# Kernel tuning notes

Measured on AMD Instinct MI355X. Metric: run time of the kernel, lower is better.

Reference implementation:

```python
import jax, jax.numpy as jnp
import numpy as np

HEAD_DIM = 128
NUM_Q_HEAD = 32
NUM_KV_HEAD = 8
GROUP_SIZE = 128
EPS = 1e-5
WINDOW = 512
CAP = 50.0
CLIP_L, CLIP_R = -0.01, 1.01
SCALE = 1.0 / np.sqrt(HEAD_DIM)
NEG = -1e9


def group_rmsnorm(x, gamma, gsz, eps):
    # x: [B, S, H]; per-group RMS over contiguous chunks of size gsz, then learned scale
    b, s, h = x.shape
    xg = x.reshape(b, s, h // gsz, gsz)
    rms = jnp.sqrt(jnp.mean(xg * xg, axis=-1, keepdims=True) + eps)
    return (xg / rms).reshape(b, s, h) * gamma


def setup_inputs() -> dict:
    key = jax.random.key(0)
    k1, k2, k3, k4, k5 = jax.random.split(key, 5)
    B, S = 2, 2048
    q = jax.random.normal(k1, (B, S, NUM_Q_HEAD, HEAD_DIM), dtype=jnp.float32)
    k = jax.random.normal(k2, (B, S, NUM_KV_HEAD, HEAD_DIM), dtype=jnp.float32)
    v = jax.random.normal(k3, (B, S, NUM_KV_HEAD, HEAD_DIM), dtype=jnp.float32)
    # GroupRMSNorm weights ~ U(init_range) = U(-1, 1)
    gamma_q = jax.random.uniform(k4, (NUM_Q_HEAD * HEAD_DIM,), dtype=jnp.float32, minval=-1.0, maxval=1.0)
    gamma_k = jax.random.uniform(k5, (NUM_KV_HEAD * HEAD_DIM,), dtype=jnp.float32, minval=-1.0, maxval=1.0)
    return {"q": q, "k": k, "v": v, "gamma_q": gamma_q, "gamma_k": gamma_k}


def reference(q, k, v, gamma_q, gamma_k):
    B, Sq, Hq, D = q.shape
    Sk, Hkv = k.shape[1], k.shape[2]
    # QK GroupRMSNorm on flattened hidden dim
    qn = group_rmsnorm(q.reshape(B, Sq, Hq * D), gamma_q, GROUP_SIZE, EPS).reshape(B, Sq, Hq, D)
    kn = group_rmsnorm(k.reshape(B, Sk, Hkv * D), gamma_k, GROUP_SIZE, EPS).reshape(B, Sk, Hkv, D)
    # GQA: repeat_interleave kv heads to match q heads
    rep = Hq // Hkv
    kr = jnp.repeat(kn, rep, axis=2)
    vr = jnp.repeat(v, rep, axis=2)
    # scores: [B, H, Sq, Sk]
    logits = jnp.einsum('bqhd,bkhd->bhqk', qn, kr) * SCALE
    # softmax capping (temperature path skipped when cap is set)
    logits = jnp.tanh(logits / CAP) * CAP
    # causal + sliding-window mask (aligned at sequence end)
    i = jnp.arange(Sq)[:, None]
    j = jnp.arange(Sk)[None, :]
    pos = i + (Sk - Sq)
    allowed = (j <= pos) & (pos - j <= WINDOW)
    logits = jnp.where(allowed, logits, NEG)
    probs = jax.nn.softmax(logits.astype(jnp.float32), axis=-1)
    # softmax clipping: clamp(probs * (r - l) + l, 0, 1)
    probs = jnp.clip(probs * (CLIP_R - CLIP_L) + CLIP_L, 0.0, 1.0)
    # output: [B, Sq, H, D]
    o = jnp.einsum('bhqk,bkhd->bqhd', probs.astype(q.dtype), vr)
    return o
```

## Files before the change

### kernel.cpp

```cpp
#include <hip/hip_runtime.h>

#define SEQ     2048
#define NQH     32
#define NKV     8
#define HD      128
#define WINDOW  512
#define QT      64
#define EPS_F   1e-5f
#define CQ2     0.12752981793f
#define PSTR    72

#define KN_OFF  0ull
#define VT_OFF  8388608ull

#define ROWPAT(r, hg) ((((r) & 3) + 8 * ((r) >> 2)) + 4 * (hg))

#define WAIT_BAR_4() asm volatile("s_waitcnt vmcnt(4)\n\ts_barrier" ::: "memory")
#define WAIT_BAR_0() asm volatile("s_waitcnt vmcnt(0)\n\ts_barrier" ::: "memory")
#define WAIT_BARL_4() asm volatile("s_waitcnt vmcnt(4) lgkmcnt(0)\n\ts_barrier" ::: "memory")
#define WAIT_BARL_0() asm volatile("s_waitcnt vmcnt(0) lgkmcnt(0)\n\ts_barrier" ::: "memory")
#define LGKM_BAR()  asm volatile("s_waitcnt lgkmcnt(0)\n\ts_barrier" ::: "memory")

using bf16x8 = __attribute__((ext_vector_type(8))) __bf16;
using f32x16 = __attribute__((ext_vector_type(16))) float;

__device__ __forceinline__ void dma16(const void* g, void* l) {
    __builtin_amdgcn_global_load_lds(
        (const __attribute__((address_space(1))) unsigned int*)g,
        (__attribute__((address_space(3))) unsigned int*)l, 16, 0, 0);
}

__global__ __launch_bounds__(256)
void prep(const float* __restrict__ k, const float* __restrict__ v,
          const float* __restrict__ gk,
          __bf16* __restrict__ kn, __bf16* __restrict__ vt)
{
    __shared__ __align__(16) __bf16 sT[HD * 72];
    const int blk = blockIdx.x;
    const int tid = threadIdx.x;
    if (blk < 512) {
        const int l16  = tid & 15;
        const int rsub = tid >> 4;
        #pragma unroll
        for (int it = 0; it < 4; it++) {
            const int row = blk * 64 + it * 16 + rsub;
            const float* src = k + (size_t)row * HD + l16 * 8;
            const float* g   = gk + (row & 7) * HD + l16 * 8;
            float4 a  = *(const float4*)(src);
            float4 b4 = *(const float4*)(src + 4);
            float ss = a.x*a.x + a.y*a.y + a.z*a.z + a.w*a.w
                     + b4.x*b4.x + b4.y*b4.y + b4.z*b4.z + b4.w*b4.w;
            ss += __shfl_xor(ss, 1); ss += __shfl_xor(ss, 2);
            ss += __shfl_xor(ss, 4); ss += __shfl_xor(ss, 8);
            const float rs = rsqrtf(ss * (1.f / 128.f) + EPS_F);
            float4 g0 = *(const float4*)(g);
            float4 g1 = *(const float4*)(g + 4);
            bf16x8 o;
            o[0] = (__bf16)(a.x  * rs * g0.x);  o[1] = (__bf16)(a.y  * rs * g0.y);
            o[2] = (__bf16)(a.z  * rs * g0.z);  o[3] = (__bf16)(a.w  * rs * g0.w);
            o[4] = (__bf16)(b4.x * rs * g1.x);  o[5] = (__bf16)(b4.y * rs * g1.y);
            o[6] = (__bf16)(b4.z * rs * g1.z);  o[7] = (__bf16)(b4.w * rs * g1.w);
            *(bf16x8*)(kn + (size_t)row * HD + l16 * 8) = o;
        }
    } else {
        const int blk2 = blk - 512;
        const int st  = blk2 & 31;
        const int kvh = (blk2 >> 5) & 7;
        const int b   = blk2 >> 8;
        const int s0  = st * 64;
        {
            const int r  = tid >> 2;
            const int q4 = tid & 3;
            const float* src = v + ((size_t)(b * SEQ + s0 + r) * NKV + kvh) * HD;
            #pragma unroll
            for (int u = 0; u < 8; u++) {
                const int d0 = q4 * 4 + u * 16;
                float4 x = *(const float4*)(src + d0);
                sT[(d0 + 0) * 72 + r] = (__bf16)x.x;
                sT[(d0 + 1) * 72 + r] = (__bf16)x.y;
                sT[(d0 + 2) * 72 + r] = (__bf16)x.z;
                sT[(d0 + 3) * 72 + r] = (__bf16)x.w;
            }
        }
        __syncthreads();
        {
            const int c     = tid & 7;
            const int dbase = tid >> 3;
            __bf16* dst = vt + ((size_t)(b * NKV + kvh) * HD) * SEQ + s0;
            #pragma unroll
            for (int i = 0; i < 4; i++) {
                const int d = dbase + i * 32;
                bf16x8 w = *(const bf16x8*)&sT[d * 72 + c * 8];
                *(bf16x8*)(dst + (size_t)d * SEQ + c * 8) = w;
            }
        }
    }
}

#define WRITEP(TTW, BUF) do {                                                  \
    _Pragma("unroll")                                                          \
    for (int half_ = 0; half_ < 2; half_++) {                                  \
        _Pragma("unroll")                                                      \
        for (int j_ = 0; j_ < 8; j_++) {                                       \
            const int r_ = half_ * 8 + j_;                                     \
            const float ee_ = (float)ec[TTW][half_][j_];                       \
            const float f_ = fminf(fmaxf(fmaf(ee_, ar[r_], -0.01f), 0.f), 1.f);\
            sP[BUF][(mhalf * 32 + ROWPAT(r_, hg)) * PSTR + krow] = (__bf16)f_; \
        }                                                                      \
    }                                                                          \
} while (0)

__global__ __launch_bounds__(256, 2)
void swa_main(const float* __restrict__ q, const __bf16* __restrict__ kn,
              const __bf16* __restrict__ vt, const float* __restrict__ gq,
              float* __restrict__ out)
{
    __shared__ __align__(16) __bf16 sKV[3][QT * HD];
    __shared__ __align__(16) __bf16 sP[2][QT * PSTR];
    __shared__ float sLp[2][QT];
    __shared__ float sInvL[QT];

    const int wg0  = blockIdx.x;
    const int xcd  = wg0 & 7;
    const int gi   = wg0 >> 3;
    const int pair = xcd * 2 + (gi >> 7);
    const int rr_  = gi & 127;
    const int qt   = rr_ & 31;
    const int h    = (pair & 7) * 4 + (rr_ >> 5);
    const int b    = pair >> 3;
    const int kvh  = pair & 7;
    const int i0   = qt * QT;
    const int tid  = threadIdx.x;
    const int lane = tid & 63;
    const int wave = tid >> 6;
    const int mhalf = wave & 1;
    const int nhalf = wave >> 1;
    const int m    = lane & 31;
    const int hg   = lane >> 5;

    const char* k_src[4];  const char* v_src[4];
    int kq_off[4];  int v_off[4];
    {
        const char* kn_head = (const char*)kn + ((size_t)b * SEQ * NKV + kvh) * 256;
        const char* vt_head = (const char*)vt + ((size_t)(b * NKV + kvh) * HD) * (SEQ * 2);
        #pragma unroll
        for (int i = 0; i < 4; i++) {
            const int chunk = wave * 4 + i;
            {
                const int r    = chunk * 4 + (lane >> 4);
                const int cpos = lane & 15;
                const int c    = (cpos & 8) | ((cpos ^ r) & 7);
                k_src[i]  = kn_head + (size_t)r * (NKV * HD * 2) + c * 16;
                kq_off[i] = chunk * 1024;
            }
            {
                const int r    = chunk * 8 + (lane >> 3);
                const int cpos = lane & 7;
                const int c    = cpos ^ (r & 7);
                v_src[i] = vt_head + (size_t)r * (SEQ * 2) + c * 16;
                v_off[i] = chunk * 1024;
            }
        }
    }

    const int t_lo   = (i0 >= WINDOW ? (i0 - WINDOW) : 0) >> 6;
    const int t_hi   = i0 >> 6;
    const int ttbias = t_hi - 8;
    const int tt0    = t_lo - ttbias;
    const int krow   = nhalf * 32 + m;
    const size_t kstride = (size_t)64 * (NKV * HD * 2);

    {
        const size_t ko = (size_t)t_lo * kstride;
        char* dst0 = (char*)&sKV[t_lo % 3][0];
        #pragma unroll
        for (int i = 0; i < 4; i++) dma16(k_src[i] + ko, dst0 + kq_off[i]);
        if (t_lo < t_hi) {
            char* dst1 = (char*)&sKV[(t_lo + 1) % 3][0];
            #pragma unroll
            for (int i = 0; i < 4; i++) dma16(k_src[i] + ko + kstride, dst1 + kq_off[i]);
        }
    }

    bf16x8 qf[8];
    {
        const int qrow = i0 + mhalf * 32 + m;
        const float* qp = q + ((size_t)(b * SEQ + qrow) * NQH + h) * HD;
        float4 qb[16];
        float ss = 0.0f;
        #pragma unroll
        for (int kf = 0; kf < 8; kf++) {
            const int d0 = kf * 16 + hg * 8;
            float4 a  = *(const float4*)(qp + d0);
            float4 b4 = *(const float4*)(qp + d0 + 4);
            qb[kf * 2] = a; qb[kf * 2 + 1] = b4;
            ss += a.x*a.x + a.y*a.y + a.z*a.z + a.w*a.w
                + b4.x*b4.x + b4.y*b4.y + b4.z*b4.z + b4.w*b4.w;
        }
        ss += __shfl_xor(ss, 32);
        const float rs = rsqrtf(ss * (1.f / 128.f) + EPS_F) * CQ2;
        const float* gp = gq + h * HD;
        #pragma unroll
        for (int kf = 0; kf < 8; kf++) {
            const int d0 = kf * 16 + hg * 8;
            float4 g0 = *(const float4*)(gp + d0);
            float4 g1 = *(const float4*)(gp + d0 + 4);
            bf16x8 f;
            f[0] = (__bf16)(qb[kf*2].x   * rs * g0.x);
            f[1] = (__bf16)(qb[kf*2].y   * rs * g0.y);
            f[2] = (__bf16)(qb[kf*2].z   * rs * g0.z);
            f[3] = (__bf16)(qb[kf*2].w   * rs * g0.w);
            f[4] = (__bf16)(qb[kf*2+1].x * rs * g1.x);
            f[5] = (__bf16)(qb[kf*2+1].y * rs * g1.y);
            f[6] = (__bf16)(qb[kf*2+1].z * rs * g1.z);
            f[7] = (__bf16)(qb[kf*2+1].w * rs * g1.w);
            qf[kf] = f;
        }
    }

    float lacc[16];
    #pragma unroll
    for (int i = 0; i < 16; i++) lacc[i] = 0.f;
    bf16x8 ec[9][2];

    #pragma unroll
    for (int tt = 0; tt < 9; tt++) {
        const int t = ttbias + tt;
        if (t >= t_lo) {
            if (t < t_hi) { WAIT_BAR_4(); } else { WAIT_BAR_0(); }
            const __bf16* kb = &sKV[t % 3][0];
            bf16x8 bk[8];
            #pragma unroll
            for (int kf = 0; kf < 8; kf++) {
                const int cc  = kf * 2 + hg;
                const int pos = (cc & 8) | ((cc ^ krow) & 7);
                bk[kf] = *(const bf16x8*)(kb + krow * HD + pos * 8);
            }
            if (t + 2 <= t_hi) {
                const size_t ko = (size_t)(t + 2) * kstride;
                char* dstp = (char*)&sKV[(t + 2) % 3][0];
                #pragma unroll
                for (int i = 0; i < 4; i++) dma16(k_src[i] + ko, dstp + kq_off[i]);
            }
            f32x16 c0, c1;
            #pragma unroll
            for (int i = 0; i < 16; i++) { c0[i] = 0.f; c1[i] = 0.f; }
            __builtin_amdgcn_s_setprio(1);
            #pragma unroll
            for (int kf = 0; kf < 4; kf++) {
                c0 = __builtin_amdgcn_mfma_f32_32x32x16_bf16(qf[2*kf],   bk[2*kf],   c0, 0, 0, 0);
                c1 = __builtin_amdgcn_mfma_f32_32x32x16_bf16(qf[2*kf+1], bk[2*kf+1], c1, 0, 0, 0);
            }
            __builtin_amdgcn_s_setprio(0);

            const bool do_mask = (t == t_hi) || (t == t_lo && i0 >= WINDOW);
            const int kj = t * 64 + krow;
            float e[16];
            #pragma unroll
            for (int r = 0; r < 16; r++) {
                float ev = __builtin_amdgcn_exp2f(c0[r] + c1[r]);
                if (do_mask) {
                    const int qi = i0 + mhalf * 32 + ROWPAT(r, hg);
                    ev = ((unsigned)(qi - kj) <= WINDOW) ? ev : 0.f;
                }
                lacc[r] += ev;
                e[r] = ev;
            }
            bf16x8 p0v, p1v;
            #pragma unroll
            for (int j = 0; j < 8; j++) { p0v[j] = (__bf16)e[j]; p1v[j] = (__bf16)e[8 + j]; }
            ec[tt][0] = p0v;  ec[tt][1] = p1v;
        }
    }

    #pragma unroll
    for (int r = 0; r < 16; r++) {
        float l = lacc[r];
        l += __shfl_xor(l, 1);  l += __shfl_xor(l, 2);  l += __shfl_xor(l, 4);
        l += __shfl_xor(l, 8);  l += __shfl_xor(l, 16);
        lacc[r] = l;
    }
    if (m == 0) {
        #pragma unroll
        for (int r = 0; r < 16; r++)
            sLp[nhalf][mhalf * 32 + ROWPAT(r, hg)] = lacc[r];
    }
    LGKM_BAR();
    {
        const size_t vo = (size_t)t_lo * 128;
        char* dst0 = (char*)&sKV[t_lo % 3][0];
        #pragma unroll
        for (int i = 0; i < 4; i++) dma16(v_src[i] + vo, dst0 + v_off[i]);
        if (t_lo < t_hi) {
            char* dst1 = (char*)&sKV[(t_lo + 1) % 3][0];
            #pragma unroll
            for (int i = 0; i < 4; i++) dma16(v_src[i] + vo + 128, dst1 + v_off[i]);
        }
    }
    if (tid < QT) sInvL[tid] = __builtin_amdgcn_rcpf(sLp[0][tid] + sLp[1][tid]);
    LGKM_BAR();

    float ar[16];
    #pragma unroll
    for (int r = 0; r < 16; r++) ar[r] = 1.02f * sInvL[mhalf * 32 + ROWPAT(r, hg)];

    #pragma unroll
    for (int tt = 0; tt < 9; tt++) if (tt == tt0) WRITEP(tt, tt & 1);

    f32x16 o0, o1;
    #pragma unroll
    for (int i = 0; i < 16; i++) { o0[i] = 0.f; o1[i] = 0.f; }

    #pragma unroll
    for (int tt = 0; tt < 9; tt++) {
        const int t = ttbias + tt;
        if (t >= t_lo) {
            if (t < t_hi) { WAIT_BARL_4(); } else { WAIT_BARL_0(); }
            const __bf16* vb = &sKV[t % 3][0];
            const __bf16* pb = &sP[tt & 1][0];
            bf16x8 pa[4], vf0[4], vf1[4];
            #pragma unroll
            for (int kf = 0; kf < 4; kf++) {
                pa[kf] = *(const bf16x8*)&pb[(mhalf * 32 + m) * PSTR + kf * 16 + hg * 8];
                const int cc = kf * 2 + hg;
                const int row0 = nhalf * 64 + m;
                const int row1 = nhalf * 64 + 32 + m;
                vf0[kf] = *(const bf16x8*)(vb + row0 * 64 + ((cc ^ row0) & 7) * 8);
                vf1[kf] = *(const bf16x8*)(vb + row1 * 64 + ((cc ^ row1) & 7) * 8);
            }
            if (t + 2 <= t_hi) {
                const size_t vo = (size_t)(t + 2) * 128;
                char* dstp = (char*)&sKV[(t + 2) % 3][0];
                #pragma unroll
                for (int i = 0; i < 4; i++) dma16(v_src[i] + vo, dstp + v_off[i]);
            }
            if (t + 1 <= t_hi) { WRITEP(tt + 1, (tt + 1) & 1); }
            __builtin_amdgcn_s_setprio(1);
            #pragma unroll
            for (int kf = 0; kf < 4; kf++) {
                o0 = __builtin_amdgcn_mfma_f32_32x32x16_bf16(pa[kf], vf0[kf], o0, 0, 0, 0);
                o1 = __builtin_amdgcn_mfma_f32_32x32x16_bf16(pa[kf], vf1[kf], o1, 0, 0, 0);
            }
            __builtin_amdgcn_s_setprio(0);
        }
    }

    #pragma unroll
    for (int r = 0; r < 16; r++) {
        const int row = i0 + mhalf * 32 + ROWPAT(r, hg);
        float* op = out + ((size_t)(b * SEQ + row) * NQH + h) * HD + nhalf * 64 + m;
        op[0]  = o0[r];
        op[32] = o1[r];
    }
}

extern "C" void kernel_launch(void* const* d_in, const int* in_sizes, int n_in,
                              void* d_out, int out_size, void* d_ws, size_t ws_size,
                              hipStream_t stream) {
    const float* q  = (const float*)d_in[0];
    const float* k  = (const float*)d_in[1];
    const float* v  = (const float*)d_in[2];
    const float* gq = (const float*)d_in[3];
    const float* gk = (const float*)d_in[4];
    float* out = (float*)d_out;

    __bf16* kn = (__bf16*)((char*)d_ws + KN_OFF);
    __bf16* vt = (__bf16*)((char*)d_ws + VT_OFF);

    prep<<<1024, 256, 0, stream>>>(k, v, gk, kn, vt);
    swa_main<<<2 * NQH * (SEQ / QT), 256, 0, stream>>>(q, kn, vt, gq, out);
}
```

Baseline: 215.6 us.

## Load K and V fragments directly from global into registers, dropping LDS staging

Replaces the triple-buffered LDS staging of K and V tiles (async global-to-LDS DMA plus waitcnt/barrier) with direct per-lane global loads into double-buffered register fragments, prefetching the next tile while computing the current one. This removes LDS traffic, most barriers, and LDS capacity use for K/V, which may allow higher occupancy. In exchange, each wave fetches its own K/V fragments with less coalesced 32-byte-strided accesses, 4 waves duplicate the loads, and register pressure rises.

```diff
diff --git a/kernel.cpp b/kernel.cpp
--- a/kernel.cpp
+++ b/kernel.cpp
@@ -15,20 +15,10 @@
 
 #define ROWPAT(r, hg) ((((r) & 3) + 8 * ((r) >> 2)) + 4 * (hg))
 
-#define WAIT_BAR_4() asm volatile("s_waitcnt vmcnt(4)\n\ts_barrier" ::: "memory")
-#define WAIT_BAR_0() asm volatile("s_waitcnt vmcnt(0)\n\ts_barrier" ::: "memory")
-#define WAIT_BARL_4() asm volatile("s_waitcnt vmcnt(4) lgkmcnt(0)\n\ts_barrier" ::: "memory")
-#define WAIT_BARL_0() asm volatile("s_waitcnt vmcnt(0) lgkmcnt(0)\n\ts_barrier" ::: "memory")
 #define LGKM_BAR()  asm volatile("s_waitcnt lgkmcnt(0)\n\ts_barrier" ::: "memory")
 
 using bf16x8 = __attribute__((ext_vector_type(8))) __bf16;
 using f32x16 = __attribute__((ext_vector_type(16))) float;
-
-__device__ __forceinline__ void dma16(const void* g, void* l) {
-    __builtin_amdgcn_global_load_lds(
-        (const __attribute__((address_space(1))) unsigned int*)g,
-        (__attribute__((address_space(3))) unsigned int*)l, 16, 0, 0);
-}
 
 __global__ __launch_bounds__(256)
 void prep(const float* __restrict__ k, const float* __restrict__ v,
@@ -97,6 +87,22 @@
     }
 }
 
+#define K_LOAD(T, DST) do {                                                    \
+    const char* p_ = kbase + (size_t)(T) * (64 * 2048);                        \
+    _Pragma("unroll")                                                          \
+    for (int kf_ = 0; kf_ < 8; kf_++)                                          \
+        DST[kf_] = *(const bf16x8*)(p_ + kf_ * 32);                            \
+} while (0)
+
+#define V_LOAD(T, DST) do {                                                    \
+    const char* p_ = vbase + (size_t)(T) * 128;                                \
+    _Pragma("unroll")                                                          \
+    for (int kf_ = 0; kf_ < 4; kf_++) {                                        \
+        DST[kf_]     = *(const bf16x8*)(p_ + kf_ * 32);                        \
+        DST[4 + kf_] = *(const bf16x8*)(p_ + 32 * (SEQ * 2) + kf_ * 32);       \
+    }                                                                          \
+} while (0)
+
 #define WRITEP(TTW, BUF) do {                                                  \
     _Pragma("unroll")                                                          \
     for (int half_ = 0; half_ < 2; half_++) {                                  \
@@ -110,12 +116,62 @@
     }                                                                          \
 } while (0)
 
+#define TILE1(TT, CUR, NXT) do {                                               \
+    const int t_ = ttbias + (TT);                                              \
+    if (t_ < t_hi) { K_LOAD(t_ + 1, NXT); }                                    \
+    f32x16 c0, c1;                                                             \
+    _Pragma("unroll")                                                          \
+    for (int i_ = 0; i_ < 16; i_++) { c0[i_] = 0.f; c1[i_] = 0.f; }            \
+    __builtin_amdgcn_s_setprio(1);                                             \
+    _Pragma("unroll")                                                          \
+    for (int kf_ = 0; kf_ < 4; kf_++) {                                        \
+        c0 = __builtin_amdgcn_mfma_f32_32x32x16_bf16(qf[2*kf_],   CUR[2*kf_],   c0, 0, 0, 0); \
+        c1 = __builtin_amdgcn_mfma_f32_32x32x16_bf16(qf[2*kf_+1], CUR[2*kf_+1], c1, 0, 0, 0); \
+    }                                                                          \
+    __builtin_amdgcn_s_setprio(0);                                             \
+    const bool do_mask_ = (t_ == t_hi) || (t_ == t_lo && i0 >= WINDOW);        \
+    const int kj_ = t_ * 64 + krow;                                            \
+    float e_[16];                                                              \
+    _Pragma("unroll")                                                          \
+    for (int r_ = 0; r_ < 16; r_++) {                                          \
+        float ev_ = __builtin_amdgcn_exp2f(c0[r_] + c1[r_]);                   \
+        if (do_mask_) {                                                        \
+            const int qi_ = i0 + mhalf * 32 + ROWPAT(r_, hg);                  \
+            ev_ = ((unsigned)(qi_ - kj_) <= WINDOW) ? ev_ : 0.f;               \
+        }                                                                      \
+        lacc[r_] += ev_;                                                       \
+        e_[r_] = ev_;                                                          \
+    }                                                                          \
+    bf16x8 p0v_, p1v_;                                                         \
+    _Pragma("unroll")                                                          \
+    for (int j_ = 0; j_ < 8; j_++) { p0v_[j_] = (__bf16)e_[j_]; p1v_[j_] = (__bf16)e_[8 + j_]; } \
+    ec[TT][0] = p0v_;  ec[TT][1] = p1v_;                                       \
+} while (0)
+
+#define TILE2(TT, CUR, NXT) do {                                               \
+    const int t_ = ttbias + (TT);                                              \
+    LGKM_BAR();                                                                \
+    const __bf16* pb_ = &sP[(TT) & 1][0];                                      \
+    bf16x8 pa_[4];                                                             \
+    _Pragma("unroll")                                                          \
+    for (int kf_ = 0; kf_ < 4; kf_++)                                          \
+        pa_[kf_] = *(const bf16x8*)&pb_[(mhalf * 32 + m) * PSTR + kf_ * 16 + hg * 8]; \
+    if (t_ < t_hi) { V_LOAD(t_ + 1, NXT); }                                    \
+    if (t_ < t_hi) { WRITEP((TT) + 1, ((TT) + 1) & 1); }                       \
+    __builtin_amdgcn_s_setprio(1);                                             \
+    _Pragma("unroll")                                                          \
+    for (int kf_ = 0; kf_ < 4; kf_++) {                                        \
+        o0 = __builtin_amdgcn_mfma_f32_32x32x16_bf16(pa_[kf_], CUR[kf_],     o0, 0, 0, 0); \
+        o1 = __builtin_amdgcn_mfma_f32_32x32x16_bf16(pa_[kf_], CUR[4 + kf_], o1, 0, 0, 0); \
+    }                                                                          \
+    __builtin_amdgcn_s_setprio(0);                                             \
+} while (0)
+
 __global__ __launch_bounds__(256, 2)
 void swa_main(const float* __restrict__ q, const __bf16* __restrict__ kn,
               const __bf16* __restrict__ vt, const float* __restrict__ gq,
               float* __restrict__ out)
 {
-    __shared__ __align__(16) __bf16 sKV[3][QT * HD];
     __shared__ __align__(16) __bf16 sP[2][QT * PSTR];
     __shared__ float sLp[2][QT];
     __shared__ float sInvL[QT];
@@ -138,48 +194,22 @@
     const int m    = lane & 31;
     const int hg   = lane >> 5;
 
-    const char* k_src[4];  const char* v_src[4];
-    int kq_off[4];  int v_off[4];
-    {
-        const char* kn_head = (const char*)kn + ((size_t)b * SEQ * NKV + kvh) * 256;
-        const char* vt_head = (const char*)vt + ((size_t)(b * NKV + kvh) * HD) * (SEQ * 2);
-        #pragma unroll
-        for (int i = 0; i < 4; i++) {
-            const int chunk = wave * 4 + i;
-            {
-                const int r    = chunk * 4 + (lane >> 4);
-                const int cpos = lane & 15;
-                const int c    = (cpos & 8) | ((cpos ^ r) & 7);
-                k_src[i]  = kn_head + (size_t)r * (NKV * HD * 2) + c * 16;
-                kq_off[i] = chunk * 1024;
-            }
-            {
-                const int r    = chunk * 8 + (lane >> 3);
-                const int cpos = lane & 7;
-                const int c    = cpos ^ (r & 7);
-                v_src[i] = vt_head + (size_t)r * (SEQ * 2) + c * 16;
-                v_off[i] = chunk * 1024;
-            }
-        }
-    }
-
     const int t_lo   = (i0 >= WINDOW ? (i0 - WINDOW) : 0) >> 6;
     const int t_hi   = i0 >> 6;
     const int ttbias = t_hi - 8;
     const int tt0    = t_lo - ttbias;
     const int krow   = nhalf * 32 + m;
-    const size_t kstride = (size_t)64 * (NKV * HD * 2);
-
-    {
-        const size_t ko = (size_t)t_lo * kstride;
-        char* dst0 = (char*)&sKV[t_lo % 3][0];
-        #pragma unroll
-        for (int i = 0; i < 4; i++) dma16(k_src[i] + ko, dst0 + kq_off[i]);
-        if (t_lo < t_hi) {
-            char* dst1 = (char*)&sKV[(t_lo + 1) % 3][0];
-            #pragma unroll
-            for (int i = 0; i < 4; i++) dma16(k_src[i] + ko + kstride, dst1 + kq_off[i]);
-        }
+
+    const char* kbase = (const char*)kn + ((size_t)b * SEQ * NKV + kvh) * 256
+                        + (size_t)krow * 2048 + hg * 16;
+    const char* vbase = (const char*)vt
+                        + ((size_t)((b * NKV + kvh) * HD) + nhalf * 64 + m) * (SEQ * 2)
+                        + hg * 16;
+
+    bf16x8 bkA[8], bkB[8];
+    #pragma unroll
+    for (int tt = 0; tt < 9; tt++) if (tt == tt0) {
+        if (tt & 1) { K_LOAD(t_lo, bkB); } else { K_LOAD(t_lo, bkA); }
     }
 
     bf16x8 qf[8];
@@ -225,51 +255,8 @@
 
     #pragma unroll
     for (int tt = 0; tt < 9; tt++) {
-        const int t = ttbias + tt;
-        if (t >= t_lo) {
-            if (t < t_hi) { WAIT_BAR_4(); } else { WAIT_BAR_0(); }
-            const __bf16* kb = &sKV[t % 3][0];
-            bf16x8 bk[8];
-            #pragma unroll
-            for (int kf = 0; kf < 8; kf++) {
-                const int cc  = kf * 2 + hg;
-                const int pos = (cc & 8) | ((cc ^ krow) & 7);
-                bk[kf] = *(const bf16x8*)(kb + krow * HD + pos * 8);
-            }
-            if (t + 2 <= t_hi) {
-                const size_t ko = (size_t)(t + 2) * kstride;
-                char* dstp = (char*)&sKV[(t + 2) % 3][0];
-                #pragma unroll
-                for (int i = 0; i < 4; i++) dma16(k_src[i] + ko, dstp + kq_off[i]);
-            }
-            f32x16 c0, c1;
-            #pragma unroll
-            for (int i = 0; i < 16; i++) { c0[i] = 0.f; c1[i] = 0.f; }
-            __builtin_amdgcn_s_setprio(1);
-            #pragma unroll
-            for (int kf = 0; kf < 4; kf++) {
-                c0 = __builtin_amdgcn_mfma_f32_32x32x16_bf16(qf[2*kf],   bk[2*kf],   c0, 0, 0, 0);
-                c1 = __builtin_amdgcn_mfma_f32_32x32x16_bf16(qf[2*kf+1], bk[2*kf+1], c1, 0, 0, 0);
-            }
-            __builtin_amdgcn_s_setprio(0);
-
-            const bool do_mask = (t == t_hi) || (t == t_lo && i0 >= WINDOW);
-            const int kj = t * 64 + krow;
-            float e[16];
-            #pragma unroll
-            for (int r = 0; r < 16; r++) {
-                float ev = __builtin_amdgcn_exp2f(c0[r] + c1[r]);
-                if (do_mask) {
-                    const int qi = i0 + mhalf * 32 + ROWPAT(r, hg);
-                    ev = ((unsigned)(qi - kj) <= WINDOW) ? ev : 0.f;
-                }
-                lacc[r] += ev;
-                e[r] = ev;
-            }
-            bf16x8 p0v, p1v;
-            #pragma unroll
-            for (int j = 0; j < 8; j++) { p0v[j] = (__bf16)e[j]; p1v[j] = (__bf16)e[8 + j]; }
-            ec[tt][0] = p0v;  ec[tt][1] = p1v;
+        if (ttbias + tt >= t_lo) {
+            if (tt & 1) { TILE1(tt, bkB, bkA); } else { TILE1(tt, bkA, bkB); }
         }
     }
 
@@ -285,27 +272,20 @@
         for (int r = 0; r < 16; r++)
             sLp[nhalf][mhalf * 32 + ROWPAT(r, hg)] = lacc[r];
     }
-    LGKM_BAR();
-    {
-        const size_t vo = (size_t)t_lo * 128;
-        char* dst0 = (char*)&sKV[t_lo % 3][0];
-        #pragma unroll
-        for (int i = 0; i < 4; i++) dma16(v_src[i] + vo, dst0 + v_off[i]);
-        if (t_lo < t_hi) {
-            char* dst1 = (char*)&sKV[(t_lo + 1) % 3][0];
-            #pragma unroll
-            for (int i = 0; i < 4; i++) dma16(v_src[i] + vo + 128, dst1 + v_off[i]);
-        }
-    }
+    __syncthreads();
     if (tid < QT) sInvL[tid] = __builtin_amdgcn_rcpf(sLp[0][tid] + sLp[1][tid]);
-    LGKM_BAR();
+    __syncthreads();
 
     float ar[16];
     #pragma unroll
     for (int r = 0; r < 16; r++) ar[r] = 1.02f * sInvL[mhalf * 32 + ROWPAT(r, hg)];
 
-    #pragma unroll
-    for (int tt = 0; tt < 9; tt++) if (tt == tt0) WRITEP(tt, tt & 1);
+    bf16x8 vfA[8], vfB[8];
+    #pragma unroll
+    for (int tt = 0; tt < 9; tt++) if (tt == tt0) {
+        if (tt & 1) { V_LOAD(t_lo, vfB); } else { V_LOAD(t_lo, vfA); }
+        WRITEP(tt, tt & 1);
+    }
 
     f32x16 o0, o1;
     #pragma unroll
@@ -313,35 +293,8 @@
 
     #pragma unroll
     for (int tt = 0; tt < 9; tt++) {
-        const int t = ttbias + tt;
-        if (t >= t_lo) {
-            if (t < t_hi) { WAIT_BARL_4(); } else { WAIT_BARL_0(); }
-            const __bf16* vb = &sKV[t % 3][0];
-            const __bf16* pb = &sP[tt & 1][0];
-            bf16x8 pa[4], vf0[4], vf1[4];
-            #pragma unroll
-            for (int kf = 0; kf < 4; kf++) {
-                pa[kf] = *(const bf16x8*)&pb[(mhalf * 32 + m) * PSTR + kf * 16 + hg * 8];
-                const int cc = kf * 2 + hg;
-                const int row0 = nhalf * 64 + m;
-                const int row1 = nhalf * 64 + 32 + m;
-                vf0[kf] = *(const bf16x8*)(vb + row0 * 64 + ((cc ^ row0) & 7) * 8);
-                vf1[kf] = *(const bf16x8*)(vb + row1 * 64 + ((cc ^ row1) & 7) * 8);
-            }
-            if (t + 2 <= t_hi) {
-                const size_t vo = (size_t)(t + 2) * 128;
-                char* dstp = (char*)&sKV[(t + 2) % 3][0];
-                #pragma unroll
-                for (int i = 0; i < 4; i++) dma16(v_src[i] + vo, dstp + v_off[i]);
-            }
-            if (t + 1 <= t_hi) { WRITEP(tt + 1, (tt + 1) & 1); }
-            __builtin_amdgcn_s_setprio(1);
-            #pragma unroll
-            for (int kf = 0; kf < 4; kf++) {
-                o0 = __builtin_amdgcn_mfma_f32_32x32x16_bf16(pa[kf], vf0[kf], o0, 0, 0, 0);
-                o1 = __builtin_amdgcn_mfma_f32_32x32x16_bf16(pa[kf], vf1[kf], o1, 0, 0, 0);
-            }
-            __builtin_amdgcn_s_setprio(0);
+        if (ttbias + tt >= t_lo) {
+            if (tt & 1) { TILE2(tt, vfB, vfA); } else { TILE2(tt, vfA, vfB); }
         }
     }
 
```

After: 275.4 us. 27.8% more time.
